# Performance work log

Hardware: AMD Instinct MI355X
Metric: run time of the kernel (lower is better)

## Reference

```python
import jax, jax.numpy as jnp
import numpy as np

N = 20000            # nodes
E = 320000           # edges (before self loops)
NUM_PLAYERS = 5000
FEAT = 64            # feature_dim
H = 128              # hidden_dim
OUT = 10             # out_features
NEG_SLOPE = 0.2


def _p(key, shape, fan_in):
    return jax.random.normal(key, shape, dtype=jnp.float32) / np.sqrt(fan_in)


def setup_inputs() -> dict:
    key = jax.random.key(0)
    ks = jax.random.split(key, 20)
    # x_player: col 0 = player id (stored as float), cols 1: = features
    ids = jax.random.randint(ks[0], (N, 1), 0, NUM_PLAYERS + 1).astype(jnp.float32)
    feats = jax.random.normal(ks[1], (N, FEAT), dtype=jnp.float32)
    x_player = jnp.concatenate([ids, feats], axis=1)
    edge_index = jax.random.randint(ks[2], (2, E), 0, N, dtype=jnp.int32)
    return {
        "x_player": x_player,
        "edge_index": edge_index,
        "emb": jax.random.normal(ks[3], (NUM_PLAYERS + 1, H), dtype=jnp.float32),
        "proj_W": _p(ks[4], (H + FEAT, H), H + FEAT),
        "proj_b": jnp.zeros((H,), jnp.float32),
        "W1l": _p(ks[5], (H, 4 * H), H),
        "W1r": _p(ks[6], (H, 4 * H), H),
        "att1": _p(ks[7], (4, H), H),
        "b1": jnp.zeros((4 * H,), jnp.float32),
        "W2l": _p(ks[8], (4 * H, H), 4 * H),
        "W2r": _p(ks[9], (4 * H, H), 4 * H),
        "att2": _p(ks[10], (1, H), H),
        "b2": jnp.zeros((H,), jnp.float32),
        "out_W": _p(ks[11], (H, OUT), H),
        "out_b": jnp.zeros((OUT,), jnp.float32),
    }


def gatv2(x, src, dst, Wl, Wr, att, bias, heads, ch, concat):
    # GATv2Conv (PyG defaults: share_weights=False, negative_slope=0.2,
    # add_self_loops handled by caller, dropout off at eval)
    xl = (x @ Wl).reshape(N, heads, ch)   # source transform (x_j)
    xr = (x @ Wr).reshape(N, heads, ch)   # target transform (x_i)
    h = xl[src] + xr[dst]                                      # [E,H,C]
    e = jnp.sum(jax.nn.leaky_relu(h, NEG_SLOPE) * att, -1)     # [E,H]
    # segment softmax over incoming edges of each dst node
    m = jax.ops.segment_max(e, dst, num_segments=N)            # [N,H]
    ex = jnp.exp(e - m[dst])
    s = jax.ops.segment_sum(ex, dst, num_segments=N)
    alpha = ex / (s[dst] + 1e-16)                              # [E,H]
    out = jax.ops.segment_sum(alpha[..., None] * xl[src], dst, num_segments=N)
    out = out.reshape(N, heads * ch) if concat else out.mean(axis=1)
    return out + bias


def reference(x_player, edge_index, emb, proj_W, proj_b,
              W1l, W1r, att1, b1, W2l, W2r, att2, b2, out_W, out_b):
    ids = x_player[:, 0].astype(jnp.int32)
    combined = jnp.concatenate([emb[ids], x_player[:, 1:]], axis=1)
    x = jax.nn.relu(combined @ proj_W + proj_b)                # [N,H]
    # add self loops (GATv2Conv default)
    loop = jnp.arange(N, dtype=edge_index.dtype)
    src = jnp.concatenate([edge_index[0], loop])
    dst = jnp.concatenate([edge_index[1], loop])
    x = jax.nn.relu(gatv2(x, src, dst, W1l, W1r, att1, b1, 4, H, True))
    x = gatv2(x, src, dst, W2l, W2r, att2, b2, 1, H, True)
    return x @ out_W + out_b                                   # [N,OUT]
```

## Files before the change

kernel.cpp:

```cpp
#include <hip/hip_runtime.h>
#include <math.h>

#define NNODES 20000
#define XP_COLS 65

typedef unsigned int uint32;
typedef __attribute__((ext_vector_type(8))) short short8;
typedef __attribute__((ext_vector_type(4))) float float4v;

__device__ __forceinline__ float bflo(uint32 u){ return __uint_as_float(u << 16); }
__device__ __forceinline__ float bfhi(uint32 u){ return __uint_as_float(u & 0xffff0000u); }
__device__ __forceinline__ unsigned short f2bf(float f){
  uint32 u = __float_as_uint(f);
  uint32 r = (u + 0x7fffu + ((u >> 16) & 1u)) >> 16;
  return (unsigned short)r;
}
__device__ __forceinline__ void unpack8(uint4 u, float* x){
  x[0]=bflo(u.x); x[1]=bfhi(u.x); x[2]=bflo(u.y); x[3]=bfhi(u.y);
  x[4]=bflo(u.z); x[5]=bfhi(u.z); x[6]=bflo(u.w); x[7]=bfhi(u.w);
}
__device__ __forceinline__ float rowsum16(float x){
  x += __int_as_float(__builtin_amdgcn_update_dpp(0, __float_as_int(x), 0x121, 0xf, 0xf, true));
  x += __int_as_float(__builtin_amdgcn_update_dpp(0, __float_as_int(x), 0x122, 0xf, 0xf, true));
  x += __int_as_float(__builtin_amdgcn_update_dpp(0, __float_as_int(x), 0x124, 0xf, 0xf, true));
  x += __int_as_float(__builtin_amdgcn_update_dpp(0, __float_as_int(x), 0x128, 0xf, 0xf, true));
  return x;
}
__device__ __forceinline__ float red64(float p){
  p = rowsum16(p);
  p += __shfl_xor(p, 16);
  p += __shfl_xor(p, 32);
  return p;
}

__global__ void k_cvt_count(const int* __restrict__ dst, int E, int* __restrict__ deg,
                            const float* __restrict__ W1l, const float* __restrict__ W1r,
                            const float* __restrict__ W2l, const float* __restrict__ W2r,
                            const float* __restrict__ projW,
                            unsigned short* __restrict__ T1l, unsigned short* __restrict__ T1r,
                            unsigned short* __restrict__ T2l, unsigned short* __restrict__ T2r,
                            unsigned short* __restrict__ Tp){
  int gid = blockIdx.x * 256 + threadIdx.x;
  if (gid < E){
    atomicAdd(&deg[dst[gid]], 1);
    return;
  }
  int idx = gid - E;
  if (idx < 65536){
    int o = idx;
    int n = o >> 7, k = o & 127;
    T1l[o] = f2bf(W1l[k * 512 + n]);
  } else if (idx < 131072){
    int o = idx - 65536;
    int n = o >> 7, k = o & 127;
    T1r[o] = f2bf(W1r[k * 512 + n]);
  } else if (idx < 196608){
    int o = idx - 131072;
    int n = o >> 9, k = o & 511;
    T2l[o] = f2bf(W2l[k * 128 + n]);
  } else if (idx < 262144){
    int o = idx - 196608;
    int n = o >> 9, k = o & 511;
    T2r[o] = f2bf(W2r[k * 128 + n]);
  } else if (idx < 286720){
    int o = idx - 262144;
    int n = o / 192, k = o - n * 192;
    Tp[o] = f2bf(projW[k * 128 + n]);
  }
}

__global__ __launch_bounds__(256) void k_scan(const int* __restrict__ deg,
                                              int* __restrict__ off,
                                              int* __restrict__ cursor){
  const int CH = 80;
  int tid = threadIdx.x;
  int lane = tid & 63, w = tid >> 6;
  int beg = tid * CH;
  bool act = beg < NNODES;
  int sum = 0;
  if (act){
    const int4* p = (const int4*)(deg + beg);
    #pragma unroll
    for (int i = 0; i < 20; i++){
      int4 v = p[i];
      sum += v.x + v.y + v.z + v.w + 4;
    }
  }
  int inc = sum;
  #pragma unroll
  for (int d = 1; d < 64; d <<= 1){
    int t = __shfl_up(inc, d, 64);
    if (lane >= d) inc += t;
  }
  __shared__ int wtot[4];
  if (lane == 63) wtot[w] = inc;
  __syncthreads();
  int wbase = 0;
  for (int i = 0; i < w; i++) wbase += wtot[i];
  int run = wbase + inc - sum;
  if (act){
    const int4* p = (const int4*)(deg + beg);
    int4* po = (int4*)(off + beg);
    int4* pc = (int4*)(cursor + beg);
    #pragma unroll
    for (int i = 0; i < 20; i++){
      int4 v = p[i];
      int4 o;
      o.x = run; run += v.x + 1;
      o.y = run; run += v.y + 1;
      o.z = run; run += v.z + 1;
      o.w = run; run += v.w + 1;
      po[i] = o; pc[i] = o;
    }
  }
  if (tid == 249) off[NNODES] = run;
}

__global__ void k_fill(const int* __restrict__ src, const int* __restrict__ dst, int E,
                       int* __restrict__ cursor, int* __restrict__ csr){
  int t = blockIdx.x * 256 + threadIdx.x;
  if (t < NNODES){
    int p = atomicAdd(&cursor[t], 1);
    csr[p] = t;
  } else if (t < NNODES + E){
    int e = t - NNODES;
    int p = atomicAdd(&cursor[dst[e]], 1);
    csr[p] = src[e];
  }
}

__global__ __launch_bounds__(256) void k_proj_mfma(const float* __restrict__ xp,
                                                   const float* __restrict__ emb,
                                                   const unsigned short* __restrict__ Bt,
                                                   const float* __restrict__ bias,
                                                   unsigned short* __restrict__ Xb){
  __shared__ unsigned short As[64][40];
  __shared__ unsigned short Bs[128][40];
  __shared__ int ids[64];
  int tid = threadIdx.x;
  int bm = blockIdx.x * 64;
  int w = tid >> 6, lane = tid & 63;
  int wm = (w >> 1) * 32, wn = (w & 1) * 64;
  int quad = lane >> 4, l16 = lane & 15;
  if (tid < 64){
    int g = bm + tid;
    ids[tid] = (g < NNODES) ? (int)xp[(size_t)g * XP_COLS] : 0;
  }
  float4v acc[2][4];
  #pragma unroll
  for (int i = 0; i < 2; i++)
    #pragma unroll
    for (int j = 0; j < 4; j++) acc[i][j] = (float4v){0.f,0.f,0.f,0.f};
  int am = tid >> 2, ak = (tid & 3) * 8;
  int gm = bm + am;
  bool mv = gm < NNODES;
  int brow = tid >> 1, bk = (tid & 1) * 16;
  __syncthreads();

  for (int k0 = 0; k0 < 192; k0 += 32){
    float v[8];
    if (k0 < 128){
      const float* ep = emb + (size_t)ids[am] * 128 + k0 + ak;
      float4 e0 = *(const float4*)ep;
      float4 e1 = *(const float4*)(ep + 4);
      v[0]=e0.x; v[1]=e0.y; v[2]=e0.z; v[3]=e0.w;
      v[4]=e1.x; v[5]=e1.y; v[6]=e1.z; v[7]=e1.w;
    } else {
      const float* fp = xp + (size_t)gm * XP_COLS + 1 + (k0 - 128) + ak;
      #pragma unroll
      for (int i = 0; i < 8; i++) v[i] = mv ? fp[i] : 0.f;
    }
    ushort4 o0, o1;
    o0.x=f2bf(v[0]); o0.y=f2bf(v[1]); o0.z=f2bf(v[2]); o0.w=f2bf(v[3]);
    o1.x=f2bf(v[4]); o1.y=f2bf(v[5]); o1.z=f2bf(v[6]); o1.w=f2bf(v[7]);
    *(ushort4*)&As[am][ak]     = o0;
    *(ushort4*)&As[am][ak + 4] = o1;
    const unsigned short* bp = Bt + (size_t)brow * 192 + k0 + bk;
    *(uint4*)&Bs[brow][bk]     = *(const uint4*)bp;
    *(uint4*)&Bs[brow][bk + 8] = *(const uint4*)(bp + 8);
    __syncthreads();
    short8 af[2], bf[4];
    #pragma unroll
    for (int t = 0; t < 2; t++) af[t] = *(const short8*)&As[wm + t * 16 + l16][quad * 8];
    #pragma unroll
    for (int t = 0; t < 4; t++) bf[t] = *(const short8*)&Bs[wn + t * 16 + l16][quad * 8];
    #pragma unroll
    for (int tm = 0; tm < 2; tm++)
      #pragma unroll
      for (int tn = 0; tn < 4; tn++)
        acc[tm][tn] = __builtin_amdgcn_mfma_f32_16x16x32_bf16(af[tm], bf[tn], acc[tm][tn], 0, 0, 0);
    __syncthreads();
  }
  #pragma unroll
  for (int tm = 0; tm < 2; tm++){
    #pragma unroll
    for (int r = 0; r < 4; r++){
      int row = bm + wm + tm * 16 + quad * 4 + r;
      if (row >= NNODES) continue;
      #pragma unroll
      for (int tn = 0; tn < 4; tn++){
        int col = wn + tn * 16 + l16;
        float val = fmaxf(acc[tm][tn][r] + bias[col], 0.f);
        Xb[(size_t)row * 128 + col] = f2bf(val);
      }
    }
  }
}

template<int K, int N, int MODE, int NH>
__global__ __launch_bounds__(256) void k_mfma(const unsigned short* __restrict__ A,
                                              const unsigned short* __restrict__ B0t,
                                              const unsigned short* __restrict__ B1t,
                                              void* __restrict__ C0, void* __restrict__ C1,
                                              const float* __restrict__ att,
                                              float* __restrict__ dl, float* __restrict__ dr,
                                              int* __restrict__ gmax){
  const unsigned short* Bt = blockIdx.z ? B1t : B0t;
  __shared__ unsigned short As[64][40];
  __shared__ unsigned short Bs[128][40];
  __shared__ float red[4][32];
  __shared__ float redu[4][32];
  int tid = threadIdx.x;
  int bm = blockIdx.y * 64;
  int bn = blockIdx.x * 128;
  int head = (NH == 1) ? 0 : blockIdx.x;
  int w = tid >> 6, lane = tid & 63;
  int wm = (w >> 1) * 32, wn = (w & 1) * 64;
  int quad = lane >> 4, l16 = lane & 15;
  float av[4], aav[4];
  #pragma unroll
  for (int tn = 0; tn < 4; tn++){
    av[tn] = att[head * 128 + wn + tn * 16 + l16];
    aav[tn] = fabsf(av[tn]);
  }
  float4v acc[2][4];
  #pragma unroll
  for (int i = 0; i < 2; i++)
    #pragma unroll
    for (int j = 0; j < 4; j++) acc[i][j] = (float4v){0.f,0.f,0.f,0.f};
  int am = tid >> 2, ak = (tid & 3) * 8;
  int gm = bm + am;
  bool mv = gm < NNODES;
  int brow = tid >> 1, bk = (tid & 1) * 16;

  for (int k0 = 0; k0 < K; k0 += 32){
    uint4 va = {0u,0u,0u,0u};
    if (mv) va = *(const uint4*)(A + (size_t)gm * K + k0 + ak);
    *(uint4*)&As[am][ak] = va;
    const unsigned short* bp = Bt + (size_t)(bn + brow) * K + k0 + bk;
    *(uint4*)&Bs[brow][bk]     = *(const uint4*)bp;
    *(uint4*)&Bs[brow][bk + 8] = *(const uint4*)(bp + 8);
    __syncthreads();
    short8 af[2], bf[4];
    #pragma unroll
    for (int t = 0; t < 2; t++) af[t] = *(const short8*)&As[wm + t * 16 + l16][quad * 8];
    #pragma unroll
    for (int t = 0; t < 4; t++) bf[t] = *(const short8*)&Bs[wn + t * 16 + l16][quad * 8];
    #pragma unroll
    for (int tm = 0; tm < 2; tm++)
      #pragma unroll
      for (int tn = 0; tn < 4; tn++)
        acc[tm][tn] = __builtin_amdgcn_mfma_f32_16x16x32_bf16(af[tm], bf[tn], acc[tm][tn], 0, 0, 0);
    __syncthreads();
  }
  #pragma unroll
  for (int tm = 0; tm < 2; tm++){
    #pragma unroll
    for (int r = 0; r < 4; r++){
      int row = bm + wm + tm * 16 + quad * 4 + r;
      if (row < NNODES){
        #pragma unroll
        for (int tn = 0; tn < 4; tn++){
          int col = bn + wn + tn * 16 + l16;
          float val = acc[tm][tn][r];
          if (MODE == 0 || blockIdx.z == 0){
            unsigned short* C = (unsigned short*)(blockIdx.z ? C1 : C0);
            C[(size_t)row * N + col] = f2bf(val);
          } else {
            ((float*)C1)[(size_t)row * N + col] = val;
          }
        }
      }
      float pd = acc[tm][0][r] * av[0];
      pd = fmaf(acc[tm][1][r], av[1], pd);
      pd = fmaf(acc[tm][2][r], av[2], pd);
      pd = fmaf(acc[tm][3][r], av[3], pd);
      float pu = fabsf(acc[tm][0][r]) * aav[0];
      pu = fmaf(fabsf(acc[tm][1][r]), aav[1], pu);
      pu = fmaf(fabsf(acc[tm][2][r]), aav[2], pu);
      pu = fmaf(fabsf(acc[tm][3][r]), aav[3], pu);
      pd = rowsum16(pd);
      pu = rowsum16(pu);
      if (l16 == 0){
        red[w][tm * 16 + quad * 4 + r]  = pd;
        redu[w][tm * 16 + quad * 4 + r] = pu;
      }
    }
  }
  __syncthreads();
  if (tid < 64){
    float vd, vu;
    if (tid < 32){ vd = red[0][tid] + red[1][tid];   vu = redu[0][tid] + redu[1][tid]; }
    else { vd = red[2][tid & 31] + red[3][tid & 31]; vu = redu[2][tid & 31] + redu[3][tid & 31]; }
    int row = bm + tid;
    bool ok = row < NNODES;
    if (ok){
      float* D = blockIdx.z ? dr : dl;
      D[row * NH + head] = vd;
    }
    if (blockIdx.z == 0){
      float v = ok ? fmaf(0.4f, vu, 0.6f * vd) : -4.0e6f;
      #pragma unroll
      for (int dd = 1; dd < 64; dd <<= 1) v = fmaxf(v, __shfl_xor(v, dd));
      if (tid == 0) atomicMax(&gmax[head], (int)ceilf(v * 256.0f) + (1 << 30));
    }
  }
}

__global__ __launch_bounds__(256) void k_attn1(const unsigned short* __restrict__ xl,
                                               const unsigned short* __restrict__ xr,
                                               const float* __restrict__ dl, const float* __restrict__ dr,
                                               const float* __restrict__ att, const float* __restrict__ bias,
                                               const int* __restrict__ gmax,
                                               const int* __restrict__ off, const int* __restrict__ csr,
                                               unsigned short* __restrict__ out){
  int tid = threadIdx.x;
  int w = tid >> 6, lane = tid & 63;
  int n = blockIdx.x;
  int h = lane >> 4;
  uint4 ur = *(const uint4*)(xr + (size_t)n * 512 + lane * 8);
  float r[8]; unpack8(ur, r);
  const float* ap = att + lane * 8;
  float4 A0 = *(const float4*)ap, A1 = *(const float4*)(ap + 4);
  float a[8] = {A0.x,A0.y,A0.z,A0.w,A1.x,A1.y,A1.z,A1.w};
  float V = 0.f;
  #pragma unroll
  for (int i = 0; i < 8; i++) V = fmaf(fabsf(a[i]), fabsf(r[i]), V);
  V = rowsum16(V);
  float Mg = (float)(gmax[h] - (1 << 30)) * (1.0f / 256.0f);
  float base = fmaf(0.6f, dr[n * 4 + h], -Mg - 0.4f * V);
  int beg = off[n], end = off[n + 1];
  int cnt = end - beg;
  int B = (cnt + 3) >> 2;

  float s = 0.f;
  float acc[8] = {0,0,0,0,0,0,0,0};
  for (int b = w; b < B; b += 4){
    int j0 = beg + b * 4;
    int i1 = j0 + 1, i2 = j0 + 2, i3 = j0 + 3;
    float m1 = 1.f, m2 = 1.f, m3 = 1.f;
    if (i1 >= end){ i1 = j0; m1 = 0.f; }
    if (i2 >= end){ i2 = j0; m2 = 0.f; }
    if (i3 >= end){ i3 = j0; m3 = 0.f; }
    int s0 = csr[j0], s1 = csr[i1], s2 = csr[i2], s3 = csr[i3];
    uint4 u0 = *(const uint4*)(xl + (size_t)s0 * 512 + lane * 8);
    uint4 u1 = *(const uint4*)(xl + (size_t)s1 * 512 + lane * 8);
    uint4 u2 = *(const uint4*)(xl + (size_t)s2 * 512 + lane * 8);
    uint4 u3 = *(const uint4*)(xl + (size_t)s3 * 512 + lane * 8);
    float d0 = dl[s0 * 4 + h], d1 = dl[s1 * 4 + h];
    float d2 = dl[s2 * 4 + h], d3 = dl[s3 * 4 + h];
    float x0[8], x1[8], x2[8], x3[8];
    unpack8(u0, x0); unpack8(u1, x1); unpack8(u2, x2); unpack8(u3, x3);
    float p0 = 0.f, p1 = 0.f, p2 = 0.f, p3 = 0.f;
    #pragma unroll
    for (int i = 0; i < 8; i++){
      p0 = fmaf(a[i], fabsf(x0[i] + r[i]), p0);
      p1 = fmaf(a[i], fabsf(x1[i] + r[i]), p1);
      p2 = fmaf(a[i], fabsf(x2[i] + r[i]), p2);
      p3 = fmaf(a[i], fabsf(x3[i] + r[i]), p3);
    }
    p0 = rowsum16(p0); p1 = rowsum16(p1); p2 = rowsum16(p2); p3 = rowsum16(p3);
    float ex0 = __expf(fmaf(0.4f, p0, fmaf(0.6f, d0, base)));
    float ex1 = __expf(fmaf(0.4f, p1, fmaf(0.6f, d1, base))) * m1;
    float ex2 = __expf(fmaf(0.4f, p2, fmaf(0.6f, d2, base))) * m2;
    float ex3 = __expf(fmaf(0.4f, p3, fmaf(0.6f, d3, base))) * m3;
    s += (ex0 + ex1) + (ex2 + ex3);
    #pragma unroll
    for (int i = 0; i < 8; i++){
      float t = fmaf(ex0, x0[i], ex1 * x1[i]);
      t = fmaf(ex2, x2[i], t);
      acc[i] = fmaf(ex3, x3[i], acc[i] + t);
    }
  }
  __shared__ float accsh[4][512];
  __shared__ float ssh[4][4];
  *(float4*)&accsh[w][lane * 8]     = make_float4(acc[0], acc[1], acc[2], acc[3]);
  *(float4*)&accsh[w][lane * 8 + 4] = make_float4(acc[4], acc[5], acc[6], acc[7]);
  if ((lane & 15) == 0) ssh[w][h] = s;
  __syncthreads();
  for (int c = tid; c < 512; c += 256){
    float v = (accsh[0][c] + accsh[1][c]) + (accsh[2][c] + accsh[3][c]);
    int hh = c >> 7;
    float sv = (ssh[0][hh] + ssh[1][hh]) + (ssh[2][hh] + ssh[3][hh]);
    float o = v / (sv + 1e-16f) + bias[c];
    out[(size_t)n * 512 + c] = f2bf(fmaxf(o, 0.f));
  }
}

__global__ __launch_bounds__(256) void k_attn2(const unsigned short* __restrict__ xl,
                                               const float* __restrict__ xr,
                                               const float* __restrict__ dl, const float* __restrict__ dr,
                                               const float* __restrict__ att, const float* __restrict__ bias,
                                               const float* __restrict__ outW, const float* __restrict__ outb,
                                               const int* __restrict__ gmax,
                                               const int* __restrict__ off, const int* __restrict__ csr,
                                               float* __restrict__ out){
  __shared__ float accsh[4][128];
  __shared__ float ssh[4];
  __shared__ float x2sh[128];
  int tid = threadIdx.x;
  int w = tid >> 6, lane = tid & 63;
  int n = blockIdx.x;
  float Wr[20];
  if (w == 0){
    const float* wp = outW + lane * 20;
    #pragma unroll
    for (int i = 0; i < 5; i++){
      float4 v = *(const float4*)(wp + i * 4);
      Wr[i*4] = v.x; Wr[i*4+1] = v.y; Wr[i*4+2] = v.z; Wr[i*4+3] = v.w;
    }
  }
  float2 rv = *(const float2*)(xr + (size_t)n * 128 + lane * 2);
  float2 av = *(const float2*)(att + lane * 2);
  float V = red64(fmaf(fabsf(av.x), fabsf(rv.x), fabsf(av.y) * fabsf(rv.y)));
  float Mg = (float)(gmax[0] - (1 << 30)) * (1.0f / 256.0f);
  float base = fmaf(0.6f, dr[n], -Mg - 0.4f * V);
  int beg = off[n], end = off[n + 1];
  int cnt = end - beg;
  int B = (cnt + 3) >> 2;
  float s = 0.f, a0 = 0.f, a1 = 0.f;
  for (int b = w; b < B; b += 4){
    int j0 = beg + b * 4;
    int i1 = j0 + 1, i2 = j0 + 2, i3 = j0 + 3;
    float m1 = 1.f, m2 = 1.f, m3 = 1.f;
    if (i1 >= end){ i1 = j0; m1 = 0.f; }
    if (i2 >= end){ i2 = j0; m2 = 0.f; }
    if (i3 >= end){ i3 = j0; m3 = 0.f; }
    int s0 = csr[j0], s1 = csr[i1], s2 = csr[i2], s3 = csr[i3];
    uint32 u0 = *(const uint32*)(xl + (size_t)s0 * 128 + lane * 2);
    uint32 u1 = *(const uint32*)(xl + (size_t)s1 * 128 + lane * 2);
    uint32 u2 = *(const uint32*)(xl + (size_t)s2 * 128 + lane * 2);
    uint32 u3 = *(const uint32*)(xl + (size_t)s3 * 128 + lane * 2);
    float d0 = dl[s0], d1 = dl[s1], d2 = dl[s2], d3 = dl[s3];
    float x00 = bflo(u0), x01 = bfhi(u0);
    float x10 = bflo(u1), x11 = bfhi(u1);
    float x20 = bflo(u2), x21 = bfhi(u2);
    float x30 = bflo(u3), x31 = bfhi(u3);
    float p0 = fmaf(av.x, fabsf(x00 + rv.x), av.y * fabsf(x01 + rv.y));
    float p1 = fmaf(av.x, fabsf(x10 + rv.x), av.y * fabsf(x11 + rv.y));
    float p2 = fmaf(av.x, fabsf(x20 + rv.x), av.y * fabsf(x21 + rv.y));
    float p3 = fmaf(av.x, fabsf(x30 + rv.x), av.y * fabsf(x31 + rv.y));
    p0 = red64(p0); p1 = red64(p1); p2 = red64(p2); p3 = red64(p3);
    float ex0 = __expf(fmaf(0.4f, p0, fmaf(0.6f, d0, base)));
    float ex1 = __expf(fmaf(0.4f, p1, fmaf(0.6f, d1, base))) * m1;
    float ex2 = __expf(fmaf(0.4f, p2, fmaf(0.6f, d2, base))) * m2;
    float ex3 = __expf(fmaf(0.4f, p3, fmaf(0.6f, d3, base))) * m3;
    s += (ex0 + ex1) + (ex2 + ex3);
    float t0 = fmaf(ex0, x00, ex1 * x10); t0 = fmaf(ex2, x20, t0);
    float t1 = fmaf(ex0, x01, ex1 * x11); t1 = fmaf(ex2, x21, t1);
    a0 = fmaf(ex3, x30, a0 + t0);
    a1 = fmaf(ex3, x31, a1 + t1);
  }
  accsh[w][lane * 2]     = a0;
  accsh[w][lane * 2 + 1] = a1;
  if (lane == 0) ssh[w] = s;
  __syncthreads();
  if (tid < 128){
    float v = (accsh[0][tid] + accsh[1][tid]) + (accsh[2][tid] + accsh[3][tid]);
    float sv = (ssh[0] + ssh[1]) + (ssh[2] + ssh[3]);
    x2sh[tid] = v / (sv + 1e-16f) + bias[tid];
  }
  __syncthreads();
  if (w == 0){
    int c = lane * 2;
    float x0 = x2sh[c], x1 = x2sh[c + 1];
    #pragma unroll
    for (int o = 0; o < 10; o++){
      float p = fmaf(x0, Wr[o], x1 * Wr[10 + o]);
      p = red64(p);
      if (lane == 0) out[(size_t)n * 10 + o] = p + outb[o];
    }
  }
}

extern "C" void kernel_launch(void* const* d_in, const int* in_sizes, int n_in,
                              void* d_out, int out_size, void* d_ws, size_t ws_size,
                              hipStream_t stream){
  const float* xp    = (const float*)d_in[0];
  const int*   ei    = (const int*)  d_in[1];
  const float* emb   = (const float*)d_in[2];
  const float* projW = (const float*)d_in[3];
  const float* projb = (const float*)d_in[4];
  const float* W1l   = (const float*)d_in[5];
  const float* W1r   = (const float*)d_in[6];
  const float* att1  = (const float*)d_in[7];
  const float* b1    = (const float*)d_in[8];
  const float* W2l   = (const float*)d_in[9];
  const float* W2r   = (const float*)d_in[10];
  const float* att2  = (const float*)d_in[11];
  const float* b2    = (const float*)d_in[12];
  const float* outW  = (const float*)d_in[13];
  const float* outb  = (const float*)d_in[14];
  float* out = (float*)d_out;

  int E = in_sizes[1] / 2;
  const int* esrc = ei;
  const int* edst = ei + E;

  char* w = (char*)d_ws;
  int* gmaxi = (int*)w; w += 32;
  int* deg  = (int*)w; w += (size_t)NNODES * 4;
  int* off  = (int*)w; w += (size_t)(NNODES + 4) * 4;
  int* cur  = (int*)w; w += (size_t)NNODES * 4;
  int* csr  = (int*)w; w += (size_t)(NNODES + E) * 4;
  unsigned short* Xb   = (unsigned short*)w; w += (size_t)NNODES * 128 * 2;
  unsigned short* Wt1l = (unsigned short*)w; w += (size_t)512 * 128 * 2;
  unsigned short* Wt1r = (unsigned short*)w; w += (size_t)512 * 128 * 2;
  unsigned short* Wt2l = (unsigned short*)w; w += (size_t)128 * 512 * 2;
  unsigned short* Wt2r = (unsigned short*)w; w += (size_t)128 * 512 * 2;
  unsigned short* Wtp  = (unsigned short*)w; w += (size_t)128 * 192 * 2;
  unsigned short* xl1b = (unsigned short*)w; w += (size_t)NNODES * 512 * 2;
  unsigned short* xr1b = (unsigned short*)w; w += (size_t)NNODES * 512 * 2;
  unsigned short* X1b  = (unsigned short*)w; w += (size_t)NNODES * 512 * 2;
  unsigned short* xl2b = (unsigned short*)w; w += (size_t)NNODES * 128 * 2;
  float* xr2 = (float*)w; w += (size_t)NNODES * 128 * 4;
  float* dl1 = (float*)w; w += (size_t)NNODES * 4 * 4;
  float* dr1 = (float*)w; w += (size_t)NNODES * 4 * 4;
  float* dl2 = (float*)w; w += (size_t)NNODES * 4;
  float* dr2 = (float*)w; w += (size_t)NNODES * 4;

  hipMemsetAsync(gmaxi, 0, 32 + (size_t)NNODES * 4, stream);
  int cvt_total = E + 286720;
  k_cvt_count<<<(cvt_total + 255) / 256, 256, 0, stream>>>(
      edst, E, deg, W1l, W1r, W2l, W2r, projW, Wt1l, Wt1r, Wt2l, Wt2r, Wtp);
  k_scan<<<1, 256, 0, stream>>>(deg, off, cur);
  k_fill<<<(NNODES + E + 255) / 256, 256, 0, stream>>>(esrc, edst, E, cur, csr);

  k_proj_mfma<<<dim3((NNODES + 63) / 64), 256, 0, stream>>>(xp, emb, Wtp, projb, Xb);
  k_mfma<128, 512, 0, 4><<<dim3(4, (NNODES + 63) / 64, 2), 256, 0, stream>>>(
      Xb, Wt1l, Wt1r, xl1b, xr1b, att1, dl1, dr1, gmaxi);
  k_attn1<<<NNODES, 256, 0, stream>>>(xl1b, xr1b, dl1, dr1, att1, b1, gmaxi, off, csr, X1b);
  k_mfma<512, 128, 1, 1><<<dim3(1, (NNODES + 63) / 64, 2), 256, 0, stream>>>(
      X1b, Wt2l, Wt2r, xl2b, xr2, att2, dl2, dr2, gmaxi + 4);
  k_attn2<<<NNODES, 256, 0, stream>>>(xl2b, xr2, dl2, dr2, att2, b2, outW, outb, gmaxi + 4, off, csr, out);
}
```

Measured before the change: 292.3 us.

## Map one wavefront per node in layer-2 attention with prefetched edge batches

```diff
diff --git a/kernel.cpp b/kernel.cpp
--- a/kernel.cpp
+++ b/kernel.cpp
@@ -397,29 +397,43 @@
   }
 }
 
-__global__ __launch_bounds__(256) void k_attn2(const unsigned short* __restrict__ xl,
-                                               const float* __restrict__ xr,
-                                               const float* __restrict__ dl, const float* __restrict__ dr,
-                                               const float* __restrict__ att, const float* __restrict__ bias,
-                                               const float* __restrict__ outW, const float* __restrict__ outb,
-                                               const int* __restrict__ gmax,
-                                               const int* __restrict__ off, const int* __restrict__ csr,
-                                               float* __restrict__ out){
-  __shared__ float accsh[4][128];
-  __shared__ float ssh[4];
-  __shared__ float x2sh[128];
+__device__ __forceinline__ void attn2_batch(const uint32* u, const float* d,
+                                            float2 rv, float2 av, float base,
+                                            float& s, float& a0, float& a1){
+  float x00 = bflo(u[0]), x01 = bfhi(u[0]);
+  float x10 = bflo(u[1]), x11 = bfhi(u[1]);
+  float x20 = bflo(u[2]), x21 = bfhi(u[2]);
+  float x30 = bflo(u[3]), x31 = bfhi(u[3]);
+  float p0 = fmaf(av.x, fabsf(x00 + rv.x), av.y * fabsf(x01 + rv.y));
+  float p1 = fmaf(av.x, fabsf(x10 + rv.x), av.y * fabsf(x11 + rv.y));
+  float p2 = fmaf(av.x, fabsf(x20 + rv.x), av.y * fabsf(x21 + rv.y));
+  float p3 = fmaf(av.x, fabsf(x30 + rv.x), av.y * fabsf(x31 + rv.y));
+  p0 = red64(p0); p1 = red64(p1); p2 = red64(p2); p3 = red64(p3);
+  float ex0 = __expf(fmaf(0.4f, p0, fmaf(0.6f, d[0], base)));
+  float ex1 = __expf(fmaf(0.4f, p1, fmaf(0.6f, d[1], base)));
+  float ex2 = __expf(fmaf(0.4f, p2, fmaf(0.6f, d[2], base)));
+  float ex3 = __expf(fmaf(0.4f, p3, fmaf(0.6f, d[3], base)));
+  s += (ex0 + ex1) + (ex2 + ex3);
+  float t0 = fmaf(ex0, x00, ex1 * x10); t0 = fmaf(ex2, x20, t0);
+  float t1 = fmaf(ex0, x01, ex1 * x11); t1 = fmaf(ex2, x21, t1);
+  a0 = fmaf(ex3, x30, a0 + t0);
+  a1 = fmaf(ex3, x31, a1 + t1);
+}
+
+__global__ __launch_bounds__(1024) void k_attn2(const unsigned short* __restrict__ xl,
+                                                const float* __restrict__ xr,
+                                                const float* __restrict__ dl, const float* __restrict__ dr,
+                                                const float* __restrict__ att, const float* __restrict__ bias,
+                                                const float* __restrict__ outW, const float* __restrict__ outb,
+                                                const int* __restrict__ gmax,
+                                                const int* __restrict__ off, const int* __restrict__ csr,
+                                                float* __restrict__ out){
+  __shared__ float Wsh[1280];
   int tid = threadIdx.x;
-  int w = tid >> 6, lane = tid & 63;
-  int n = blockIdx.x;
-  float Wr[20];
-  if (w == 0){
-    const float* wp = outW + lane * 20;
-    #pragma unroll
-    for (int i = 0; i < 5; i++){
-      float4 v = *(const float4*)(wp + i * 4);
-      Wr[i*4] = v.x; Wr[i*4+1] = v.y; Wr[i*4+2] = v.z; Wr[i*4+3] = v.w;
-    }
-  }
+  for (int i = tid; i < 1280; i += 1024) Wsh[i] = outW[i];
+  __syncthreads();
+  int lane = tid & 63;
+  int n = blockIdx.x * 16 + (tid >> 6);
   float2 rv = *(const float2*)(xr + (size_t)n * 128 + lane * 2);
   float2 av = *(const float2*)(att + lane * 2);
   float V = red64(fmaf(fabsf(av.x), fabsf(rv.x), fabsf(av.y) * fabsf(rv.y)));
@@ -427,59 +441,55 @@
   float base = fmaf(0.6f, dr[n], -Mg - 0.4f * V);
   int beg = off[n], end = off[n + 1];
   int cnt = end - beg;
-  int B = (cnt + 3) >> 2;
-  float s = 0.f, a0 = 0.f, a1 = 0.f;
-  for (int b = w; b < B; b += 4){
-    int j0 = beg + b * 4;
-    int i1 = j0 + 1, i2 = j0 + 2, i3 = j0 + 3;
-    float m1 = 1.f, m2 = 1.f, m3 = 1.f;
-    if (i1 >= end){ i1 = j0; m1 = 0.f; }
-    if (i2 >= end){ i2 = j0; m2 = 0.f; }
-    if (i3 >= end){ i3 = j0; m3 = 0.f; }
-    int s0 = csr[j0], s1 = csr[i1], s2 = csr[i2], s3 = csr[i3];
-    uint32 u0 = *(const uint32*)(xl + (size_t)s0 * 128 + lane * 2);
-    uint32 u1 = *(const uint32*)(xl + (size_t)s1 * 128 + lane * 2);
-    uint32 u2 = *(const uint32*)(xl + (size_t)s2 * 128 + lane * 2);
-    uint32 u3 = *(const uint32*)(xl + (size_t)s3 * 128 + lane * 2);
-    float d0 = dl[s0], d1 = dl[s1], d2 = dl[s2], d3 = dl[s3];
-    float x00 = bflo(u0), x01 = bfhi(u0);
-    float x10 = bflo(u1), x11 = bfhi(u1);
-    float x20 = bflo(u2), x21 = bfhi(u2);
-    float x30 = bflo(u3), x31 = bfhi(u3);
-    float p0 = fmaf(av.x, fabsf(x00 + rv.x), av.y * fabsf(x01 + rv.y));
-    float p1 = fmaf(av.x, fabsf(x10 + rv.x), av.y * fabsf(x11 + rv.y));
-    float p2 = fmaf(av.x, fabsf(x20 + rv.x), av.y * fabsf(x21 + rv.y));
-    float p3 = fmaf(av.x, fabsf(x30 + rv.x), av.y * fabsf(x31 + rv.y));
-    p0 = red64(p0); p1 = red64(p1); p2 = red64(p2); p3 = red64(p3);
-    float ex0 = __expf(fmaf(0.4f, p0, fmaf(0.6f, d0, base)));
-    float ex1 = __expf(fmaf(0.4f, p1, fmaf(0.6f, d1, base))) * m1;
-    float ex2 = __expf(fmaf(0.4f, p2, fmaf(0.6f, d2, base))) * m2;
-    float ex3 = __expf(fmaf(0.4f, p3, fmaf(0.6f, d3, base))) * m3;
-    s += (ex0 + ex1) + (ex2 + ex3);
-    float t0 = fmaf(ex0, x00, ex1 * x10); t0 = fmaf(ex2, x20, t0);
-    float t1 = fmaf(ex0, x01, ex1 * x11); t1 = fmaf(ex2, x21, t1);
-    a0 = fmaf(ex3, x30, a0 + t0);
-    a1 = fmaf(ex3, x31, a1 + t1);
-  }
-  accsh[w][lane * 2]     = a0;
-  accsh[w][lane * 2 + 1] = a1;
-  if (lane == 0) ssh[w] = s;
-  __syncthreads();
-  if (tid < 128){
-    float v = (accsh[0][tid] + accsh[1][tid]) + (accsh[2][tid] + accsh[3][tid]);
-    float sv = (ssh[0] + ssh[1]) + (ssh[2] + ssh[3]);
-    x2sh[tid] = v / (sv + 1e-16f) + bias[tid];
-  }
-  __syncthreads();
-  if (w == 0){
-    int c = lane * 2;
-    float x0 = x2sh[c], x1 = x2sh[c + 1];
-    #pragma unroll
-    for (int o = 0; o < 10; o++){
-      float p = fmaf(x0, Wr[o], x1 * Wr[10 + o]);
-      p = red64(p);
-      if (lane == 0) out[(size_t)n * 10 + o] = p + outb[o];
-    }
+  int nfull = cnt >> 2;
+  float s = 0.f;
+  float a0 = 0.f, a1 = 0.f;
+  uint32 uA[4], uB[4];
+  float dA[4], dB[4];
+  int j = beg;
+  if (nfull > 0){
+    int s0 = csr[j], s1 = csr[j+1], s2 = csr[j+2], s3 = csr[j+3];
+    uA[0] = *(const uint32*)(xl + (size_t)s0 * 128 + lane * 2);
+    uA[1] = *(const uint32*)(xl + (size_t)s1 * 128 + lane * 2);
+    uA[2] = *(const uint32*)(xl + (size_t)s2 * 128 + lane * 2);
+    uA[3] = *(const uint32*)(xl + (size_t)s3 * 128 + lane * 2);
+    dA[0] = dl[s0]; dA[1] = dl[s1]; dA[2] = dl[s2]; dA[3] = dl[s3];
+  }
+  for (int b = 0; b < nfull; b++){
+    int jn = j + 4;
+    if (b + 1 < nfull){
+      int s0 = csr[jn], s1 = csr[jn+1], s2 = csr[jn+2], s3 = csr[jn+3];
+      uB[0] = *(const uint32*)(xl + (size_t)s0 * 128 + lane * 2);
+      uB[1] = *(const uint32*)(xl + (size_t)s1 * 128 + lane * 2);
+      uB[2] = *(const uint32*)(xl + (size_t)s2 * 128 + lane * 2);
+      uB[3] = *(const uint32*)(xl + (size_t)s3 * 128 + lane * 2);
+      dB[0] = dl[s0]; dB[1] = dl[s1]; dB[2] = dl[s2]; dB[3] = dl[s3];
+    }
+    attn2_batch(uA, dA, rv, av, base, s, a0, a1);
+    j = jn;
+    #pragma unroll
+    for (int i = 0; i < 4; i++){ uA[i] = uB[i]; dA[i] = dB[i]; }
+  }
+  for (; j < end; j++){
+    int sn = csr[j];
+    float dls = dl[sn];
+    uint32 u = *(const uint32*)(xl + (size_t)sn * 128 + lane * 2);
+    float x0 = bflo(u), x1 = bfhi(u);
+    float p = red64(fmaf(av.x, fabsf(x0 + rv.x), av.y * fabsf(x1 + rv.y)));
+    float ex = __expf(fmaf(0.4f, p, fmaf(0.6f, dls, base)));
+    s += ex;
+    a0 = fmaf(ex, x0, a0);
+    a1 = fmaf(ex, x1, a1);
+  }
+  float inv = 1.f / (s + 1e-16f);
+  int c = lane * 2;
+  float x2_0 = fmaf(a0, inv, bias[c]);
+  float x2_1 = fmaf(a1, inv, bias[c + 1]);
+  #pragma unroll
+  for (int o = 0; o < 10; o++){
+    float p = fmaf(x2_0, Wsh[c * 10 + o], x2_1 * Wsh[(c + 1) * 10 + o]);
+    p = red64(p);
+    if (lane == 0) out[(size_t)n * 10 + o] = p + outb[o];
   }
 }
 
@@ -542,5 +552,5 @@
   k_attn1<<<NNODES, 256, 0, stream>>>(xl1b, xr1b, dl1, dr1, att1, b1, gmaxi, off, csr, X1b);
   k_mfma<512, 128, 1, 1><<<dim3(1, (NNODES + 63) / 64, 2), 256, 0, stream>>>(
       X1b, Wt2l, Wt2r, xl2b, xr2, att2, dl2, dr2, gmaxi + 4);
-  k_attn2<<<NNODES, 256, 0, stream>>>(xl2b, xr2, dl2, dr2, att2, b2, outW, outb, gmaxi + 4, off, csr, out);
-}
+  k_attn2<<<NNODES / 16, 1024, 0, stream>>>(xl2b, xr2, dl2, dr2, att2, b2, outW, outb, gmaxi + 4, off, csr, out);
+}
```

Measured after the change: 286.8 us. No clear change (-1.9%).
